# Kernel optimization log

Hardware: AMD Instinct MI355X
Metric: run time of the kernel (lower is better)

The kernel has to match this reference:

```python
import jax, jax.numpy as jnp
import numpy as np

N_UP, N_DOWN, N_NUC = 32, 32, 16
N_ELEC = N_UP + N_DOWN
N_PART = N_ELEC + N_NUC
L = 3            # n_interactions
BASIS = 32
K = 128          # kernel_dim
D = 128          # embedding_dim
BS = 256


def ssp(x):
    # shifted softplus: softplus(x) - log 2
    return jax.nn.softplus(x) - jnp.log(2.0).astype(x.dtype)


def setup_inputs() -> dict:
    key = jax.random.key(0)
    ks = jax.random.split(key, 14)
    s = 0.05
    dists_basis = jax.random.normal(ks[0], (BS, N_ELEC, N_PART, BASIS), jnp.float32)
    # electron embedding: one shared row per spin channel, materialized as full table
    e_up = jax.random.normal(ks[1], (D,), jnp.float32)
    e_dn = jax.random.normal(ks[2], (D,), jnp.float32)
    embedding_elec = jnp.concatenate([
        jnp.broadcast_to(e_up, (N_UP, D)),
        jnp.broadcast_to(e_dn, (N_DOWN, D)),
    ], axis=0)
    embedding_nuc = jax.random.normal(ks[3], (N_NUC, K), jnp.float32)
    # per-interaction params, stacked on leading layer dim (weights stored as (in, out))
    return {
        'dists_basis': dists_basis,
        'embedding_elec': embedding_elec,
        'embedding_nuc': embedding_nuc,
        'kW1': jax.random.normal(ks[4], (L, BASIS, K), jnp.float32) * s,
        'kb1': jnp.zeros((L, K), jnp.float32),
        'kW2': jax.random.normal(ks[5], (L, K, K), jnp.float32) * s,
        'kb2': jnp.zeros((L, K), jnp.float32),
        'eiW': jax.random.normal(ks[6], (L, D, K), jnp.float32) * s,
        'eoW1': jax.random.normal(ks[7], (L, K, D), jnp.float32) * s,
        'eob1': jnp.zeros((L, D), jnp.float32),
        'eoW2': jax.random.normal(ks[8], (L, D, D), jnp.float32) * s,
        'eob2': jnp.zeros((L, D), jnp.float32),
    }


def reference(dists_basis, embedding_elec, embedding_nuc, kW1, kb1, kW2, kb2, eiW, eoW1, eob1, eoW2, eob2):
    bs, n_elec, n_part, _ = dists_basis.shape
    # ZeroDiagKernel mask: zero electron-electron self pairs (i == j < n_elec)
    diag = jnp.pad(jnp.eye(n_elec, dtype=dists_basis.dtype), ((0, 0), (0, n_part - n_elec)))
    mask = (1.0 - diag)[None, :, :, None]
    xs = jnp.broadcast_to(embedding_elec, (bs,) + embedding_elec.shape)  # (bs, n_elec, D)
    nuc = jnp.broadcast_to(embedding_nuc, (bs,) + embedding_nuc.shape)   # (bs, n_nuc, K)
    for l in range(kW1.shape[0]):
        # filter-generating MLP on distance basis -> (bs, n_elec, n_part, K)
        Ws = ssp(jnp.einsum('bijf,fk->bijk', dists_basis, kW1[l]) + kb1[l])
        Ws = (jnp.einsum('bijk,km->bijm', Ws, kW2[l]) + kb2[l]) * mask
        zs = jnp.einsum('bid,dk->bik', xs, eiW[l])          # embed_in, no bias
        zs = jnp.concatenate([zs, nuc], axis=1)              # (bs, n_part, K)
        zs = jnp.einsum('bijk,bjk->bik', Ws, zs)             # cfconv aggregation
        out = jnp.einsum('bik,kd->bid', ssp(jnp.einsum('bik,kd->bid', zs, eoW1[l]) + eob1[l]), eoW2[l]) + eob2[l]
        xs = xs + out
    return xs
```

## Files before the change

### kernel.cpp

```cpp
#include <hip/hip_runtime.h>

#define NBS    256
#define NELEC  64
#define NPART  80
#define NBASIS 32
#define KD     128
#define DD     128
#define IB     8

#define LOG2E 1.4426950408889634f
#define LN2   0.69314718055994530942f

typedef short v8s __attribute__((ext_vector_type(8)));
typedef float v4f __attribute__((ext_vector_type(4)));
typedef __bf16 bf2 __attribute__((ext_vector_type(2)));

#if __has_builtin(__builtin_amdgcn_exp2f)
#define EXP2F(x) __builtin_amdgcn_exp2f(x)
#else
#define EXP2F(x) __expf((x) * LN2)
#endif
#if __has_builtin(__builtin_amdgcn_logf)
#define LOG2F(x) __builtin_amdgcn_logf(x)
#else
#define LOG2F(x) __log2f(x)
#endif

__device__ __forceinline__ float sspf2(float y) {
    float t = 1.0f + EXP2F(y);
    return __builtin_fmaf(LOG2F(t), LN2, -LN2);
}

__device__ __forceinline__ float bf2f(unsigned short u) {
    unsigned int x = ((unsigned int)u) << 16;
    return __builtin_bit_cast(float, x);
}
__device__ __forceinline__ unsigned short f2bf(float f) {
    return __builtin_bit_cast(unsigned short, (__bf16)f);
}
__device__ __forceinline__ unsigned int pk2(float lo, float hi) {
    bf2 p;
    p.x = (__bf16)lo;
    p.y = (__bf16)hi;
    return __builtin_bit_cast(unsigned int, p);
}

__global__ __launch_bounds__(256) void k_init_xs(const float* __restrict__ emb,
                                                 float* __restrict__ xs,
                                                 unsigned short* __restrict__ xs_bf) {
    int idx = blockIdx.x * 256 + threadIdx.x;
    float v = emb[idx & (NELEC * DD - 1)];
    xs[idx] = v;
    xs_bf[idx] = f2bf(v);
}

__global__ __launch_bounds__(256) void k_nuc(const float* __restrict__ nuc,
                                             unsigned short* __restrict__ zsbf) {
    int idx = blockIdx.x * 256 + threadIdx.x;
    int b = idx >> 11;
    int rem = idx & 2047;
    zsbf[(size_t)b * (NPART * KD) + NELEC * KD + rem] = f2bf(nuc[rem]);
}

__global__ __launch_bounds__(256) void k_prep(const float* __restrict__ kW1g,
                                              const float* __restrict__ kW2g,
                                              unsigned short* __restrict__ kW1Tf,
                                              unsigned short* __restrict__ kW2Tf) {
    const int l = blockIdx.x;
    const int t = threadIdx.x;
    for (int e = 0; e < 64; ++e) {
        int o = e * 256 + t;
        int mt = o >> 11, ks = (o >> 9) & 3, lane = (o >> 3) & 63, jj = o & 7;
        int q = lane >> 4, cc = lane & 15;
        int kf = ks * 32 + q * 8 + jj;
        int kcol = mt * 16 + cc;
        kW2Tf[(size_t)l * 16384 + o] = f2bf(kW2g[(size_t)l * 16384 + kf * 128 + kcol]);
    }
    for (int e = 0; e < 16; ++e) {
        int o = e * 256 + t;
        int kct = o >> 9, lane = (o >> 3) & 63, jj = o & 7;
        int q = lane >> 4, cc = lane & 15;
        int f = q * 8 + jj;
        int kcol = kct * 16 + cc;
        kW1Tf[(size_t)l * 4096 + o] = f2bf(kW1g[(size_t)l * 4096 + f * 128 + kcol] * LOG2E);
    }
}

__global__ __launch_bounds__(256) void k_prep_w(const float* __restrict__ eiW,
                                                const float* __restrict__ eoW1,
                                                const float* __restrict__ eoW2,
                                                unsigned short* __restrict__ Wf) {
    const int bi = blockIdx.x;
    const int which = bi / 3, l = bi % 3;
    const float* src = (which == 0 ? eiW : which == 1 ? eoW1 : eoW2) + (size_t)l * 16384;
    unsigned short* dst = Wf + (size_t)bi * 16384;
    const float s = (which == 1) ? LOG2E : 1.0f;
    const int t = threadIdx.x;
    for (int e = 0; e < 64; ++e) {
        int o = e * 256 + t;
        int mt = o >> 11, ks = (o >> 9) & 3, lane = (o >> 3) & 63, jj = o & 7;
        int q = lane >> 4, cc = lane & 15;
        dst[o] = f2bf(src[(ks * 32 + q * 8 + jj) * 128 + mt * 16 + cc] * s);
    }
}

__global__ __launch_bounds__(256) void k_prep_misc(const float* __restrict__ kb1,
                                                   const float* __restrict__ kb2,
                                                   float* __restrict__ kb1f,
                                                   float* __restrict__ kb2f) {
    const int t = threadIdx.x;
    for (int o = t; o < 3 * 4 * 64 * 8; o += 256) {
        int l = o >> 11, rem = o & 2047;
        int w = rem >> 9, lane = (rem >> 3) & 63, e = o & 7;
        int mt = e >> 2, r = e & 3, q = lane >> 4;
        int kcol = (2 * w + mt) * 16 + q * 4 + r;
        kb1f[o] = kb1[l * 128 + kcol] * LOG2E;
        kb2f[o] = kb2[l * 128 + kcol];
    }
}

template <int MODE>
__global__ __launch_bounds__(256) void k_gemm(
    const unsigned short* __restrict__ Xbf,
    const unsigned short* __restrict__ Wf,
    const float* __restrict__ bias,
    unsigned short* __restrict__ Obf,
    float* __restrict__ Of,
    int ostride) {
    const int blk = blockIdx.x;
    const int b = blk >> 1, kh2 = blk & 1;
    const int t = threadIdx.x, lane = t & 63, w = t >> 6;
    const int q = lane >> 4, c = lane & 15;

    const unsigned short* xb = Xbf + (size_t)b * (NELEC * KD);
    v8s A[4];
#pragma unroll
    for (int ks = 0; ks < 4; ++ks)
        A[ks] = *(const v8s*)(xb + (w * 16 + c) * 128 + ks * 32 + q * 8);

#pragma unroll
    for (int kt = 0; kt < 4; ++kt) {
        const int n0 = kh2 * 64 + kt * 16;
        float bv = (MODE >= 1) ? bias[n0 + c] : 0.0f;
        if (MODE == 1) bv *= LOG2E;
        v4f acc = {bv, bv, bv, bv};
#pragma unroll
        for (int ks = 0; ks < 4; ++ks) {
            v8s B = *(const v8s*)(Wf + (((size_t)(kh2 * 4 + kt) * 4 + ks) * 64 + lane) * 8);
            acc = __builtin_amdgcn_mfma_f32_16x16x32_bf16(A[ks], B, acc, 0, 0, 0);
        }
#pragma unroll
        for (int r = 0; r < 4; ++r) {
            float v = acc[r];
            if (MODE == 1) v = sspf2(v);
            int row = w * 16 + q * 4 + r, col = n0 + c;
            if (MODE == 2) {
                size_t o = (size_t)b * (NELEC * KD) + row * 128 + col;
                float nv = Of[o] + v;
                Of[o] = nv;
                Obf[o] = f2bf(nv);
            } else {
                Obf[(size_t)b * ostride + row * 128 + col] = f2bf(v);
            }
        }
    }
}

__global__ __launch_bounds__(256, 2) void k_cfconv_mfma(
    const float* __restrict__ dists,
    const float* __restrict__ kb1f, const float* __restrict__ kb2f,
    const unsigned short* __restrict__ zsbf,
    const unsigned short* __restrict__ kW1Tf,
    const unsigned short* __restrict__ kW2Tf,
    unsigned short* __restrict__ aggbf, int l) {
    __shared__ __align__(16) unsigned short s_dists[2560];
    __shared__ __align__(16) unsigned short s_X1[10240];

    const int blk = blockIdx.x;
    const int b = blk >> 3;
    const int ig = blk & 7;
    const int t = threadIdx.x;
    const int lane = t & 63;
    const int w = t >> 6;
    const int q = lane >> 4;
    const int c = lane & 15;

    v8s a1[2], a2[2][4];
    {
        const uint4* w1p = (const uint4*)kW1Tf;
        const uint4* w2p = (const uint4*)kW2Tf;
#pragma unroll
        for (int t1 = 0; t1 < 2; ++t1) {
            uint4 u = w1p[(l * 8 + 2 * w + t1) * 64 + lane];
            a1[t1] = __builtin_bit_cast(v8s, u);
        }
#pragma unroll
        for (int mt = 0; mt < 2; ++mt)
#pragma unroll
            for (int ks = 0; ks < 4; ++ks) {
                uint4 u = w2p[((l * 8 + 2 * w + mt) * 4 + ks) * 64 + lane];
                a2[mt][ks] = __builtin_bit_cast(v8s, u);
            }
    }
    float4 kb1v[2], kb2v[2];
    {
        const float4* p1 = (const float4*)(kb1f + ((size_t)(l * 4 + w) * 64 + lane) * 8);
        kb1v[0] = p1[0];
        kb1v[1] = p1[1];
        const float4* p2 = (const float4*)(kb2f + ((size_t)(l * 4 + w) * 64 + lane) * 8);
        kb2v[0] = p2[0];
        kb2v[1] = p2[1];
    }
    float zf[2][5][4];
    {
        const unsigned short* zb = zsbf + (size_t)b * (NPART * KD) + w * 32 + q * 4;
#pragma unroll
        for (int mt = 0; mt < 2; ++mt)
#pragma unroll
            for (int jt = 0; jt < 5; ++jt) {
                ushort4 zv = *(const ushort4*)(zb + (jt * 16 + c) * 128 + mt * 16);
                zf[mt][jt][0] = bf2f(zv.x);
                zf[mt][jt][1] = bf2f(zv.y);
                zf[mt][jt][2] = bf2f(zv.z);
                zf[mt][jt][3] = bf2f(zv.w);
            }
    }

    const float* dbase = dists + ((size_t)b * NELEC + ig * IB) * (NPART * NBASIS);

#pragma unroll 1
    for (int ii = 0; ii < IB; ++ii) {
        const int i = ig * IB + ii;

        {
            const float* dg = dbase + (size_t)ii * (NPART * NBASIS);
            for (int jt = w; jt < 5; jt += 4) {
                const float* dj = dg + (jt * 16 + c) * 32 + q * 8;
                float4 v0 = *(const float4*)dj;
                float4 v1 = *(const float4*)(dj + 4);
                uint4 pk;
                pk.x = pk2(v0.x, v0.y);
                pk.y = pk2(v0.z, v0.w);
                pk.z = pk2(v1.x, v1.y);
                pk.w = pk2(v1.z, v1.w);
                *(uint4*)(s_dists + (jt * 64 + lane) * 8) = pk;
            }
        }
        __syncthreads();

#pragma unroll
        for (int jt = 0; jt < 5; ++jt) {
            v8s bd = *(const v8s*)(s_dists + (jt * 64 + lane) * 8);
#pragma unroll
            for (int t1 = 0; t1 < 2; ++t1) {
                v4f d = {kb1v[t1].x, kb1v[t1].y, kb1v[t1].z, kb1v[t1].w};
                d = __builtin_amdgcn_mfma_f32_16x16x32_bf16(a1[t1], bd, d, 0, 0, 0);
                uint2 o;
                o.x = pk2(sspf2(d[0]), sspf2(d[1]));
                o.y = pk2(sspf2(d[2]), sspf2(d[3]));
                int qB = 2 * t1 + (q >> 1);
                *(uint2*)(s_X1 + ((jt * 4 + w) * 64 + qB * 16 + c) * 8 + (q & 1) * 4) = o;
            }
        }
        __syncthreads();

        v4f acc[2][5];
#pragma unroll
        for (int mt = 0; mt < 2; ++mt)
#pragma unroll
            for (int jt = 0; jt < 5; ++jt)
                acc[mt][jt] = (v4f){(&kb2v[mt].x)[0], (&kb2v[mt].x)[1],
                                    (&kb2v[mt].x)[2], (&kb2v[mt].x)[3]};

#pragma unroll
        for (int jt = 0; jt < 5; ++jt) {
#pragma unroll
            for (int ks = 0; ks < 4; ++ks) {
                v8s bx = *(const v8s*)(s_X1 + ((jt * 4 + ks) * 64 + lane) * 8);
                acc[0][jt] = __builtin_amdgcn_mfma_f32_16x16x32_bf16(a2[0][ks], bx, acc[0][jt], 0, 0, 0);
                acc[1][jt] = __builtin_amdgcn_mfma_f32_16x16x32_bf16(a2[1][ks], bx, acc[1][jt], 0, 0, 0);
            }
        }

        float red[8];
#pragma unroll
        for (int v = 0; v < 8; ++v) red[v] = 0.0f;
        const int jt_i = i >> 4;
        const bool lanehit = (c == (i & 15));
#pragma unroll
        for (int jt = 0; jt < 5; ++jt) {
            if (jt == jt_i) {
#pragma unroll
                for (int mt = 0; mt < 2; ++mt)
#pragma unroll
                    for (int r = 0; r < 4; ++r) {
                        float a = lanehit ? 0.0f : acc[mt][jt][r];
                        red[mt * 4 + r] += a * zf[mt][jt][r];
                    }
            } else {
#pragma unroll
                for (int mt = 0; mt < 2; ++mt)
#pragma unroll
                    for (int r = 0; r < 4; ++r)
                        red[mt * 4 + r] += acc[mt][jt][r] * zf[mt][jt][r];
            }
        }

        float vals[8];
#pragma unroll
        for (int v = 0; v < 8; ++v) vals[v] = red[v];
#pragma unroll
        for (int B = 0; B < 3; ++B) {
            const int off = 1 << B;
            const bool up = (c >> B) & 1;
#pragma unroll
            for (int k2 = 0; k2 < (4 >> B); ++k2) {
                float aa = vals[2 * k2], bb = vals[2 * k2 + 1];
                float mine = up ? bb : aa;
                float other = up ? aa : bb;
                vals[k2] = mine + __shfl_xor(other, off, 64);
            }
        }
        float x = vals[0] + __shfl_xor(vals[0], 8, 64);

        if (c < 8) {
            int kcol = w * 32 + ((c >> 2) & 1) * 16 + q * 4 + (c & 3);
            aggbf[((size_t)b * NELEC + i) * 128 + kcol] = f2bf(x);
        }
    }
}

extern "C" void kernel_launch(void* const* d_in, const int* in_sizes, int n_in,
                              void* d_out, int out_size, void* d_ws, size_t ws_size,
                              hipStream_t stream) {
    const float* dists = (const float*)d_in[0];
    const float* emb_e = (const float*)d_in[1];
    const float* emb_n = (const float*)d_in[2];
    const float* kW1   = (const float*)d_in[3];
    const float* kb1   = (const float*)d_in[4];
    const float* kW2   = (const float*)d_in[5];
    const float* kb2   = (const float*)d_in[6];
    const float* eiW   = (const float*)d_in[7];
    const float* eoW1  = (const float*)d_in[8];
    const float* eob1  = (const float*)d_in[9];
    const float* eoW2  = (const float*)d_in[10];
    const float* eob2  = (const float*)d_in[11];

    float* xs = (float*)d_out;
    unsigned short* zsbf  = (unsigned short*)d_ws;
    unsigned short* aggbf = zsbf + NBS * NPART * KD;
    unsigned short* hbf   = aggbf + NBS * NELEC * KD;
    unsigned short* xs_bf = hbf + NBS * NELEC * KD;
    unsigned short* kW1Tf = xs_bf + NBS * NELEC * KD;
    unsigned short* kW2Tf = kW1Tf + 3 * 4096;
    unsigned short* Wf    = kW2Tf + 3 * 16384;
    float* kb1f = (float*)(Wf + 9 * 16384);
    float* kb2f = kb1f + 3 * 4 * 64 * 8;

    k_init_xs<<<(NBS * NELEC * DD) / 256, 256, 0, stream>>>(emb_e, xs, xs_bf);
    k_prep<<<3, 256, 0, stream>>>(kW1, kW2, kW1Tf, kW2Tf);
    k_prep_w<<<9, 256, 0, stream>>>(eiW, eoW1, eoW2, Wf);
    k_prep_misc<<<1, 256, 0, stream>>>(kb1, kb2, kb1f, kb2f);
    k_nuc<<<(NBS * 16 * KD) / 256, 256, 0, stream>>>(emb_n, zsbf);

    for (int l = 0; l < 3; ++l) {
        k_gemm<0><<<NBS * 2, 256, 0, stream>>>(
            xs_bf, Wf + (size_t)(0 * 3 + l) * 16384, nullptr, zsbf, nullptr, NPART * KD);

        k_cfconv_mfma<<<NBS * (NELEC / IB), 256, 0, stream>>>(
            dists, kb1f, kb2f, zsbf, kW1Tf, kW2Tf, aggbf, l);

        k_gemm<1><<<NBS * 2, 256, 0, stream>>>(
            aggbf, Wf + (size_t)(1 * 3 + l) * 16384, eob1 + l * DD, hbf, nullptr, NELEC * KD);

        k_gemm<2><<<NBS * 2, 256, 0, stream>>>(
            hbf, Wf + (size_t)(2 * 3 + l) * 16384, eob2 + l * DD, xs_bf, xs, NELEC * KD);
    }
}
```

Measured before the change: 543.6 us.

## Fuse per-layer output MLP and next embed_in into one kernel; prefetch dists

Adds a k_tail kernel that runs the embed_out MLP (two GEMMs plus ssp), the residual update and the next layer's embed_in GEMM in one block per batch element. Intermediates stay in shared memory instead of going through global bf16 buffers, which removes launches and global round-trips. Separately, the cfconv kernel now prefetches the next electron's distance rows into registers while the current one is being computed, so global load latency overlaps with MFMA work. The trade-off is 512-thread blocks with a large shared tile, which may lower occupancy, and the extra register pressure from the prefetch.

```diff
diff --git a/kernel.cpp b/kernel.cpp
--- a/kernel.cpp
+++ b/kernel.cpp
@@ -166,6 +166,106 @@
     }
 }
 
+template <int LAST>
+__global__ __launch_bounds__(512) void k_tail(
+    const unsigned short* __restrict__ aggbf,
+    const unsigned short* __restrict__ WfA,
+    const float* __restrict__ b1,
+    const unsigned short* __restrict__ WfB,
+    const float* __restrict__ b2,
+    const unsigned short* __restrict__ WfC,
+    float* __restrict__ xs,
+    unsigned short* __restrict__ xs_bf,
+    unsigned short* __restrict__ zsbf) {
+    __shared__ float hl[64 * 129];
+    const int b = blockIdx.x;
+    const int t = threadIdx.x, lane = t & 63, w = t >> 6;
+    const int wr = w & 3, kh = w >> 2;
+    const int q = lane >> 4, c = lane & 15;
+
+    const unsigned short* ab = aggbf + (size_t)b * (NELEC * KD);
+    v8s A[4];
+#pragma unroll
+    for (int ks = 0; ks < 4; ++ks)
+        A[ks] = *(const v8s*)(ab + (wr * 16 + c) * 128 + ks * 32 + q * 8);
+
+#pragma unroll
+    for (int kt2 = 0; kt2 < 4; ++kt2) {
+        const int kt = kh * 4 + kt2;
+        float bv = b1[kt * 16 + c] * LOG2E;
+        v4f acc = {bv, bv, bv, bv};
+#pragma unroll
+        for (int ks = 0; ks < 4; ++ks) {
+            v8s B = *(const v8s*)(WfA + (((size_t)kt * 4 + ks) * 64 + lane) * 8);
+            acc = __builtin_amdgcn_mfma_f32_16x16x32_bf16(A[ks], B, acc, 0, 0, 0);
+        }
+#pragma unroll
+        for (int r = 0; r < 4; ++r)
+            hl[(wr * 16 + q * 4 + r) * 129 + kt * 16 + c] = sspf2(acc[r]);
+    }
+    __syncthreads();
+#pragma unroll
+    for (int ks = 0; ks < 4; ++ks) {
+        const float* hp = hl + (wr * 16 + c) * 129 + ks * 32 + q * 8;
+        uint4 u;
+        u.x = pk2(hp[0], hp[1]);
+        u.y = pk2(hp[2], hp[3]);
+        u.z = pk2(hp[4], hp[5]);
+        u.w = pk2(hp[6], hp[7]);
+        A[ks] = __builtin_bit_cast(v8s, u);
+    }
+    __syncthreads();
+
+    float* xb = xs + (size_t)b * (NELEC * DD);
+    unsigned short* xbb = xs_bf + (size_t)b * (NELEC * DD);
+#pragma unroll
+    for (int kt2 = 0; kt2 < 4; ++kt2) {
+        const int kt = kh * 4 + kt2;
+        float bv = b2[kt * 16 + c];
+        v4f acc = {bv, bv, bv, bv};
+#pragma unroll
+        for (int ks = 0; ks < 4; ++ks) {
+            v8s B = *(const v8s*)(WfB + (((size_t)kt * 4 + ks) * 64 + lane) * 8);
+            acc = __builtin_amdgcn_mfma_f32_16x16x32_bf16(A[ks], B, acc, 0, 0, 0);
+        }
+#pragma unroll
+        for (int r = 0; r < 4; ++r) {
+            int row = wr * 16 + q * 4 + r, col = kt * 16 + c;
+            float nv = xb[row * 128 + col] + acc[r];
+            xb[row * 128 + col] = nv;
+            xbb[row * 128 + col] = f2bf(nv);
+            if (!LAST) hl[row * 129 + col] = nv;
+        }
+    }
+    if (!LAST) {
+        __syncthreads();
+#pragma unroll
+        for (int ks = 0; ks < 4; ++ks) {
+            const float* hp = hl + (wr * 16 + c) * 129 + ks * 32 + q * 8;
+            uint4 u;
+            u.x = pk2(hp[0], hp[1]);
+            u.y = pk2(hp[2], hp[3]);
+            u.z = pk2(hp[4], hp[5]);
+            u.w = pk2(hp[6], hp[7]);
+            A[ks] = __builtin_bit_cast(v8s, u);
+        }
+        unsigned short* zb = zsbf + (size_t)b * (NPART * KD);
+#pragma unroll
+        for (int kt2 = 0; kt2 < 4; ++kt2) {
+            const int kt = kh * 4 + kt2;
+            v4f acc = {0.0f, 0.0f, 0.0f, 0.0f};
+#pragma unroll
+            for (int ks = 0; ks < 4; ++ks) {
+                v8s B = *(const v8s*)(WfC + (((size_t)kt * 4 + ks) * 64 + lane) * 8);
+                acc = __builtin_amdgcn_mfma_f32_16x16x32_bf16(A[ks], B, acc, 0, 0, 0);
+            }
+#pragma unroll
+            for (int r = 0; r < 4; ++r)
+                zb[(wr * 16 + q * 4 + r) * 128 + kt * 16 + c] = f2bf(acc[r]);
+        }
+    }
+}
+
 __global__ __launch_bounds__(256, 2) void k_cfconv_mfma(
     const float* __restrict__ dists,
     const float* __restrict__ kb1f, const float* __restrict__ kb2f,
@@ -228,25 +328,46 @@
 
     const float* dbase = dists + ((size_t)b * NELEC + ig * IB) * (NPART * NBASIS);
 
+    float4 p0a, p0b, p1a, p1b;
+    {
+        const float* dj = dbase + (w * 16 + c) * 32 + q * 8;
+        p0a = *(const float4*)dj;
+        p0b = *(const float4*)(dj + 4);
+        if (w == 0) {
+            const float* dj4 = dbase + (64 + c) * 32 + q * 8;
+            p1a = *(const float4*)dj4;
+            p1b = *(const float4*)(dj4 + 4);
+        }
+    }
+    {
+        uint4 pk;
+        pk.x = pk2(p0a.x, p0a.y); pk.y = pk2(p0a.z, p0a.w);
+        pk.z = pk2(p0b.x, p0b.y); pk.w = pk2(p0b.z, p0b.w);
+        *(uint4*)(s_dists + (w * 64 + lane) * 8) = pk;
+        if (w == 0) {
+            uint4 pk4;
+            pk4.x = pk2(p1a.x, p1a.y); pk4.y = pk2(p1a.z, p1a.w);
+            pk4.z = pk2(p1b.x, p1b.y); pk4.w = pk2(p1b.z, p1b.w);
+            *(uint4*)(s_dists + (4 * 64 + lane) * 8) = pk4;
+        }
+    }
+
 #pragma unroll 1
     for (int ii = 0; ii < IB; ++ii) {
         const int i = ig * IB + ii;
-
-        {
-            const float* dg = dbase + (size_t)ii * (NPART * NBASIS);
-            for (int jt = w; jt < 5; jt += 4) {
-                const float* dj = dg + (jt * 16 + c) * 32 + q * 8;
-                float4 v0 = *(const float4*)dj;
-                float4 v1 = *(const float4*)(dj + 4);
-                uint4 pk;
-                pk.x = pk2(v0.x, v0.y);
-                pk.y = pk2(v0.z, v0.w);
-                pk.z = pk2(v1.x, v1.y);
-                pk.w = pk2(v1.z, v1.w);
-                *(uint4*)(s_dists + (jt * 64 + lane) * 8) = pk;
-            }
-        }
         __syncthreads();
+
+        if (ii + 1 < IB) {
+            const float* dg = dbase + (size_t)(ii + 1) * (NPART * NBASIS);
+            const float* dj = dg + (w * 16 + c) * 32 + q * 8;
+            p0a = *(const float4*)dj;
+            p0b = *(const float4*)(dj + 4);
+            if (w == 0) {
+                const float* dj4 = dg + (64 + c) * 32 + q * 8;
+                p1a = *(const float4*)dj4;
+                p1b = *(const float4*)(dj4 + 4);
+            }
+        }
 
 #pragma unroll
         for (int jt = 0; jt < 5; ++jt) {
@@ -263,6 +384,19 @@
             }
         }
         __syncthreads();
+
+        if (ii + 1 < IB) {
+            uint4 pk;
+            pk.x = pk2(p0a.x, p0a.y); pk.y = pk2(p0a.z, p0a.w);
+            pk.z = pk2(p0b.x, p0b.y); pk.w = pk2(p0b.z, p0b.w);
+            *(uint4*)(s_dists + (w * 64 + lane) * 8) = pk;
+            if (w == 0) {
+                uint4 pk4;
+                pk4.x = pk2(p1a.x, p1a.y); pk4.y = pk2(p1a.z, p1a.w);
+                pk4.z = pk2(p1b.x, p1b.y); pk4.w = pk2(p1b.z, p1b.w);
+                *(uint4*)(s_dists + (4 * 64 + lane) * 8) = pk4;
+            }
+        }
 
         v4f acc[2][5];
 #pragma unroll
@@ -363,17 +497,27 @@
     k_prep_misc<<<1, 256, 0, stream>>>(kb1, kb2, kb1f, kb2f);
     k_nuc<<<(NBS * 16 * KD) / 256, 256, 0, stream>>>(emb_n, zsbf);
 
+    k_gemm<0><<<NBS * 2, 256, 0, stream>>>(
+        xs_bf, Wf + (size_t)(0 * 3 + 0) * 16384, nullptr, zsbf, nullptr, NPART * KD);
+
     for (int l = 0; l < 3; ++l) {
-        k_gemm<0><<<NBS * 2, 256, 0, stream>>>(
-            xs_bf, Wf + (size_t)(0 * 3 + l) * 16384, nullptr, zsbf, nullptr, NPART * KD);
-
         k_cfconv_mfma<<<NBS * (NELEC / IB), 256, 0, stream>>>(
             dists, kb1f, kb2f, zsbf, kW1Tf, kW2Tf, aggbf, l);
 
-        k_gemm<1><<<NBS * 2, 256, 0, stream>>>(
-            aggbf, Wf + (size_t)(1 * 3 + l) * 16384, eob1 + l * DD, hbf, nullptr, NELEC * KD);
-
-        k_gemm<2><<<NBS * 2, 256, 0, stream>>>(
-            hbf, Wf + (size_t)(2 * 3 + l) * 16384, eob2 + l * DD, xs_bf, xs, NELEC * KD);
-    }
-}
+        if (l < 2) {
+            k_tail<0><<<NBS, 512, 0, stream>>>(
+                aggbf,
+                Wf + (size_t)(1 * 3 + l) * 16384, eob1 + l * DD,
+                Wf + (size_t)(2 * 3 + l) * 16384, eob2 + l * DD,
+                Wf + (size_t)(0 * 3 + (l + 1)) * 16384,
+                xs, xs_bf, zsbf);
+        } else {
+            k_tail<1><<<NBS, 512, 0, stream>>>(
+                aggbf,
+                Wf + (size_t)(1 * 3 + l) * 16384, eob1 + l * DD,
+                Wf + (size_t)(2 * 3 + l) * 16384, eob2 + l * DD,
+                nullptr,
+                xs, xs_bf, zsbf);
+        }
+    }
+}
```

Result: faster. 525.6 us (-3.3%).
